# Performance work log

Hardware: AMD Instinct MI355X
Metric: run time of the kernel (lower is better)

The kernel has to match this reference:

```python
import jax, jax.numpy as jnp
import numpy as np

NUM_HEADS = 16


def setup_inputs() -> dict:
    key = jax.random.key(0)
    ks = jax.random.split(key, 5)
    b, s, d = 2, 2048, 1024
    std = (2.0 / (d + d)) ** 0.5
    x = jax.random.normal(ks[0], (b, s, d), dtype=jnp.float32)
    Wq = jax.random.normal(ks[1], (d, d), dtype=jnp.float32) * std
    Wk = jax.random.normal(ks[2], (d, d), dtype=jnp.float32) * std
    Wv = jax.random.normal(ks[3], (d, d), dtype=jnp.float32) * std
    Wo = jax.random.normal(ks[4], (d, d), dtype=jnp.float32) * std
    return {"x": x, "Wq": Wq, "Wk": Wk, "Wv": Wv, "Wo": Wo}


def reference(x, Wq, Wk, Wv, Wo):
    b, s, d = x.shape
    h = NUM_HEADS
    dk = d // h
    # projections: bias-free x @ W (W is [in, out])
    def split_heads(t):
        return t.reshape(b, s, h, dk).transpose(0, 2, 1, 3)  # b h s dk
    q = split_heads(x @ Wq)
    k = split_heads(x @ Wk)
    v = split_heads(x @ Wv)
    scale = 1.0 / jnp.sqrt(jnp.asarray(dk, dtype=x.dtype))
    scores = jnp.einsum('bhqd,bhkd->bhqk', q, k) * scale  # b h s s
    causal = jnp.tril(jnp.ones((s, s), dtype=bool))
    scores = jnp.where(causal, scores, -jnp.inf)
    probs = jax.nn.softmax(scores, axis=-1)
    out = jnp.einsum('bhqk,bhkd->bhqd', probs, v)
    out = out.transpose(0, 2, 1, 3).reshape(b, s, d)  # b s (h dk)
    return out @ Wo
```

## Files before the change

kernel.cpp:

```cpp
#include <hip/hip_runtime.h>

typedef unsigned short u16;
typedef unsigned int   u32;

using bf16x8 = __attribute__((ext_vector_type(8))) __bf16;
using bf16x4 = __attribute__((ext_vector_type(4))) __bf16;
using f32x4  = __attribute__((ext_vector_type(4))) float;
using s16x4  = __attribute__((ext_vector_type(4))) short;

#define NH    16
#define DKH   64
#define SEQ   2048
#define BAT   2
#define DMOD  1024

#define QSCALE 0.18033688011112042f

__device__ __forceinline__ u16 f2bf(float f) {
  union { float f; u32 u; } v; v.f = f;
  u32 r = v.u + 0x7fffu + ((v.u >> 16) & 1u);
  return (u16)(r >> 16);
}

__device__ __forceinline__ u32 pack2bf(float a, float b) {
  union { float f; u32 u; } x, y; x.f = a; y.f = b;
  u32 ua = x.u + 0x7fffu + ((x.u >> 16) & 1u);
  u32 ub = y.u + 0x7fffu + ((y.u >> 16) & 1u);
  return __builtin_amdgcn_perm(ub, ua, 0x07060302u);
}

__device__ __forceinline__ s16x4 pk4bf(float a, float b, float c, float d) {
  union { bf16x4 bv; s16x4 sv; } u;
  u.bv[0] = (__bf16)a; u.bv[1] = (__bf16)b; u.bv[2] = (__bf16)c; u.bv[3] = (__bf16)d;
  return u.sv;
}

#if __has_builtin(__builtin_amdgcn_exp2f)
#define EXP2(x) __builtin_amdgcn_exp2f(x)
#else
#define EXP2(x) exp2f(x)
#endif

#if __has_builtin(__builtin_amdgcn_mfma_f32_16x16x16bf16_1k)
__device__ __forceinline__ f32x4 mfma16(s16x4 a, s16x4 b, f32x4 c) {
  return __builtin_amdgcn_mfma_f32_16x16x16bf16_1k(a, b, c, 0, 0, 0);
}
#else
__device__ __forceinline__ f32x4 mfma16(s16x4 a, s16x4 b, f32x4 c) {
  f32x4 d;
  asm volatile("v_mfma_f32_16x16x16_bf16 %0, %1, %2, %3\n\ts_nop 7\n\ts_nop 7"
               : "=v"(d) : "v"(a), "v"(b), "v"(c));
  return d;
}
#endif

__global__ __launch_bounds__(256) void transpose_all(const float* __restrict__ Wq,
                                                     const float* __restrict__ Wk,
                                                     const float* __restrict__ Wv,
                                                     const float* __restrict__ Wo,
                                                     u16* __restrict__ Wt) {
  __shared__ u16 t[32][33];
  const float* W = blockIdx.z == 0 ? Wq : blockIdx.z == 1 ? Wk : blockIdx.z == 2 ? Wv : Wo;
  u16* o = Wt + (size_t)blockIdx.z * DMOD * DMOD;
  int bx = blockIdx.x * 32, by = blockIdx.y * 32;
  int x = threadIdx.x, y = threadIdx.y;
  #pragma unroll
  for (int i = 0; i < 32; i += 8)
    t[y + i][x] = f2bf(W[(size_t)(by + y + i) * DMOD + bx + x]);
  __syncthreads();
  #pragma unroll
  for (int i = 0; i < 32; i += 8)
    o[(size_t)(bx + y + i) * DMOD + by + x] = t[x][y + i];
}

__global__ __launch_bounds__(256) void convert_x(const float* __restrict__ x,
                                                 u16* __restrict__ xb) {
  size_t i = ((size_t)blockIdx.x * 256 + threadIdx.x) * 8;
  float4 f0 = *(const float4*)(x + i);
  float4 f1 = *(const float4*)(x + i + 4);
  uint4 o;
  o.x = pack2bf(f0.x, f0.y); o.y = pack2bf(f0.z, f0.w);
  o.z = pack2bf(f1.x, f1.y); o.w = pack2bf(f1.z, f1.w);
  *(uint4*)(xb + i) = o;
}

__global__ __launch_bounds__(256, 3) void gemm_qkv(const u16* __restrict__ A,
                                                   const u16* __restrict__ Bt,
                                                   u16* __restrict__ Qo,
                                                   u16* __restrict__ Ko,
                                                   u16* __restrict__ Vo) {
  __shared__ __align__(16) u16 As[128 * 40];
  __shared__ __align__(16) u16 Bs[128 * 40];
  const int tid  = threadIdx.x;
  const int lane = tid & 63, wv = tid >> 6;
  const int wm   = wv >> 1, wn = wv & 1;
  const int lrow = lane & 15, quad = lane >> 4;
  const int tileM = blockIdx.x * 128, tileN = blockIdx.y * 128;
  const int r0 = tid >> 2, c0 = (tid & 3) * 8;
  const int r1 = r0 + 64;

  const f32x4 fz = {0.f, 0.f, 0.f, 0.f};
  f32x4 acc[4][4];
  #pragma unroll
  for (int i = 0; i < 4; ++i)
    #pragma unroll
    for (int j = 0; j < 4; ++j) acc[i][j] = fz;

  uint4 a0 = *(const uint4*)(&A [(size_t)(tileM + r0) * DMOD + c0]);
  uint4 a1 = *(const uint4*)(&A [(size_t)(tileM + r1) * DMOD + c0]);
  uint4 b0 = *(const uint4*)(&Bt[(size_t)(tileN + r0) * DMOD + c0]);
  uint4 b1 = *(const uint4*)(&Bt[(size_t)(tileN + r1) * DMOD + c0]);

  for (int kt = 0; kt < DMOD; kt += 32) {
    __syncthreads();
    *(uint4*)(&As[r0 * 40 + c0]) = a0;
    *(uint4*)(&As[r1 * 40 + c0]) = a1;
    *(uint4*)(&Bs[r0 * 40 + c0]) = b0;
    *(uint4*)(&Bs[r1 * 40 + c0]) = b1;
    if (kt + 32 < DMOD) {
      a0 = *(const uint4*)(&A [(size_t)(tileM + r0) * DMOD + kt + 32 + c0]);
      a1 = *(const uint4*)(&A [(size_t)(tileM + r1) * DMOD + kt + 32 + c0]);
      b0 = *(const uint4*)(&Bt[(size_t)(tileN + r0) * DMOD + kt + 32 + c0]);
      b1 = *(const uint4*)(&Bt[(size_t)(tileN + r1) * DMOD + kt + 32 + c0]);
    }
    __syncthreads();
    bf16x8 af[4], bfr[4];
    #pragma unroll
    for (int mt = 0; mt < 4; ++mt)
      af[mt] = *(const bf16x8*)(&As[(wm * 64 + mt * 16 + lrow) * 40 + quad * 8]);
    #pragma unroll
    for (int nt = 0; nt < 4; ++nt)
      bfr[nt] = *(const bf16x8*)(&Bs[(wn * 64 + nt * 16 + lrow) * 40 + quad * 8]);
    #pragma unroll
    for (int mt = 0; mt < 4; ++mt)
      #pragma unroll
      for (int nt = 0; nt < 4; ++nt)
        acc[mt][nt] = __builtin_amdgcn_mfma_f32_16x16x32_bf16(af[mt], bfr[nt],
                                                              acc[mt][nt], 0, 0, 0);
  }

  #pragma unroll
  for (int mt = 0; mt < 4; ++mt) {
    #pragma unroll
    for (int nt = 0; nt < 4; ++nt) {
      int gm0 = tileM + wm * 64 + mt * 16 + quad * 4;
      int gn  = tileN + wn * 64 + nt * 16 + lrow;
      int which = gn >> 10, col = gn & 1023;
      int bb = gm0 >> 11, srw0 = gm0 & (SEQ - 1);
      int hh = col >> 6, dki = col & (DKH - 1);
      size_t bhi = (size_t)(bb * NH + hh);
      if (which == 0) {
        #pragma unroll
        for (int r = 0; r < 4; ++r)
          Qo[(bhi * SEQ + srw0 + r) * DKH + dki] = f2bf(acc[mt][nt][r] * QSCALE);
      } else if (which == 1) {
        #pragma unroll
        for (int r = 0; r < 4; ++r)
          Ko[(bhi * SEQ + srw0 + r) * DKH + dki] = f2bf(acc[mt][nt][r]);
      } else {
        uint2 pk;
        pk.x = pack2bf(acc[mt][nt][0], acc[mt][nt][1]);
        pk.y = pack2bf(acc[mt][nt][2], acc[mt][nt][3]);
        *(uint2*)(&Vo[(((bhi * (SEQ / 4)) + (srw0 >> 2)) * DKH + dki) * 4]) = pk;
      }
    }
  }
}

__global__ __launch_bounds__(256, 3) void gemm_out(const u16* __restrict__ A,
                                                   const u16* __restrict__ Bt,
                                                   float* __restrict__ Co) {
  __shared__ __align__(16) u16 As[128 * 40];
  __shared__ __align__(16) u16 Bs[64 * 40];
  const int tid  = threadIdx.x;
  const int lane = tid & 63, wv = tid >> 6;
  const int wm   = wv & 1, wn = wv >> 1;
  const int lrow = lane & 15, quad = lane >> 4;
  const int tileM = blockIdx.x * 128, tileN = blockIdx.y * 64;
  const int r0 = tid >> 2, c0 = (tid & 3) * 8;
  const int r1 = r0 + 64;

  const f32x4 fz = {0.f, 0.f, 0.f, 0.f};
  f32x4 acc[4][2];
  #pragma unroll
  for (int i = 0; i < 4; ++i) { acc[i][0] = fz; acc[i][1] = fz; }

  uint4 a0 = *(const uint4*)(&A [(size_t)(tileM + r0) * DMOD + c0]);
  uint4 a1 = *(const uint4*)(&A [(size_t)(tileM + r1) * DMOD + c0]);
  uint4 b0 = *(const uint4*)(&Bt[(size_t)(tileN + (r0 & 63)) * DMOD + c0]);

  for (int kt = 0; kt < DMOD; kt += 32) {
    __syncthreads();
    *(uint4*)(&As[r0 * 40 + c0]) = a0;
    *(uint4*)(&As[r1 * 40 + c0]) = a1;
    if (r0 < 64) *(uint4*)(&Bs[r0 * 40 + c0]) = b0;
    if (kt + 32 < DMOD) {
      a0 = *(const uint4*)(&A [(size_t)(tileM + r0) * DMOD + kt + 32 + c0]);
      a1 = *(const uint4*)(&A [(size_t)(tileM + r1) * DMOD + kt + 32 + c0]);
      b0 = *(const uint4*)(&Bt[(size_t)(tileN + (r0 & 63)) * DMOD + kt + 32 + c0]);
    }
    __syncthreads();
    bf16x8 af[4], bfr[2];
    #pragma unroll
    for (int mt = 0; mt < 4; ++mt)
      af[mt] = *(const bf16x8*)(&As[(wm * 64 + mt * 16 + lrow) * 40 + quad * 8]);
    #pragma unroll
    for (int nt = 0; nt < 2; ++nt)
      bfr[nt] = *(const bf16x8*)(&Bs[(wn * 32 + nt * 16 + lrow) * 40 + quad * 8]);
    #pragma unroll
    for (int mt = 0; mt < 4; ++mt)
      #pragma unroll
      for (int nt = 0; nt < 2; ++nt)
        acc[mt][nt] = __builtin_amdgcn_mfma_f32_16x16x32_bf16(af[mt], bfr[nt],
                                                              acc[mt][nt], 0, 0, 0);
  }

  #pragma unroll
  for (int mt = 0; mt < 4; ++mt)
    #pragma unroll
    for (int nt = 0; nt < 2; ++nt)
      #pragma unroll
      for (int r = 0; r < 4; ++r) {
        int gm = tileM + wm * 64 + mt * 16 + quad * 4 + r;
        int gn = tileN + wn * 32 + nt * 16 + lrow;
        Co[(size_t)gm * DMOD + gn] = acc[mt][nt][r];
      }
}

#define KP 72
#define VP 132
#define OP 68

__global__ __launch_bounds__(128, 2) void attn_k(const u16* __restrict__ Q,
                                                 const u16* __restrict__ Kg,
                                                 const u16* __restrict__ Vg,
                                                 u16* __restrict__ Og) {
  __shared__ __align__(16) u16 Ks[128 * KP];
  __shared__ __align__(16) u16 Vs[64 * VP];

  const int tid  = threadIdx.x;
  const int lane = tid & 63, w = tid >> 6;
  const int lrow = lane & 15, quad = lane >> 4;
  const int bh = blockIdx.x;
  const int t  = blockIdx.y;
  const int qb = (t < 16) ? t : 47 - t;
  const int b = bh >> 4, h = bh & 15;
  const int jmax = qb >> 1;
  const int qoff = qb & 1;

  const u16* Qbh = Q  + (size_t)bh * SEQ * DKH;
  const u16* Kbh = Kg + (size_t)bh * SEQ * DKH;
  const u16* Vbh = Vg + (size_t)bh * SEQ * DKH;

  bf16x8 bq[2][2];
  #pragma unroll
  for (int s = 0; s < 2; ++s)
    #pragma unroll
    for (int kk = 0; kk < 2; ++kk)
      bq[s][kk] = *(const bf16x8*)(&Qbh[(size_t)(qb * 64 + (2 * w + s) * 16 + lrow) * DKH
                                        + kk * 32 + quad * 8]);

  uint4 kreg[8], vreg[8];
  #pragma unroll
  for (int k = 0; k < 8; ++k) {
    int ci = k * 128 + tid;
    kreg[k] = *(const uint4*)(&Kbh[(size_t)(ci >> 3) * DKH + (ci & 7) * 8]);
    vreg[k] = *(const uint4*)(&Vbh[(size_t)(ci >> 5) * 256 + (ci & 31) * 8]);
  }

  const f32x4 fz = {0.f, 0.f, 0.f, 0.f};
  f32x4 oacc[2][4];
  #pragma unroll
  for (int s = 0; s < 2; ++s)
    #pragma unroll
    for (int d = 0; d < 4; ++d) oacc[s][d] = fz;
  float lsum[2] = {0.f, 0.f};

  for (int j = 0; j <= jmax; ++j) {
    if (j) __syncthreads();

    #pragma unroll
    for (int k = 0; k < 8; ++k) {
      int ci = k * 128 + tid;
      *(uint4*)(&Ks[(ci >> 3) * KP + (ci & 7) * 8]) = kreg[k];
      int sq = ci >> 5, dkp = ci & 31;
      union { uint4 q; uint2 d[2]; } vv; vv.q = vreg[k];
      *(uint2*)(&Vs[(2 * dkp)     * VP + 4 * sq]) = vv.d[0];
      *(uint2*)(&Vs[(2 * dkp + 1) * VP + 4 * sq]) = vv.d[1];
    }

    if (j < jmax) {
      const int jn = j + 1;
      #pragma unroll
      for (int k = 0; k < 8; ++k) {
        int ci = k * 128 + tid;
        kreg[k] = *(const uint4*)(&Kbh[(size_t)(jn * 128 + (ci >> 3)) * DKH + (ci & 7) * 8]);
        vreg[k] = *(const uint4*)(&Vbh[(size_t)(jn * 32 + (ci >> 5)) * 256 + (ci & 31) * 8]);
      }
    }

    __syncthreads();

    if (j < jmax) {
      f32x4 sacc[2][8];
      #pragma unroll
      for (int s = 0; s < 2; ++s)
        #pragma unroll
        for (int m = 0; m < 8; ++m) sacc[s][m] = fz;
      #pragma unroll
      for (int kk = 0; kk < 2; ++kk)
        #pragma unroll
        for (int m = 0; m < 8; ++m) {
          bf16x8 ak = *(const bf16x8*)(&Ks[(m * 16 + lrow) * KP + kk * 32 + quad * 8]);
          sacc[0][m] = __builtin_amdgcn_mfma_f32_16x16x32_bf16(ak, bq[0][kk], sacc[0][m], 0, 0, 0);
          sacc[1][m] = __builtin_amdgcn_mfma_f32_16x16x32_bf16(ak, bq[1][kk], sacc[1][m], 0, 0, 0);
        }
      #pragma unroll
      for (int m = 0; m < 8; ++m) {
        float p00 = EXP2(sacc[0][m][0]), p01 = EXP2(sacc[0][m][1]);
        float p02 = EXP2(sacc[0][m][2]), p03 = EXP2(sacc[0][m][3]);
        float p10 = EXP2(sacc[1][m][0]), p11 = EXP2(sacc[1][m][1]);
        float p12 = EXP2(sacc[1][m][2]), p13 = EXP2(sacc[1][m][3]);
        lsum[0] += (p00 + p01) + (p02 + p03);
        lsum[1] += (p10 + p11) + (p12 + p13);
        s16x4 pk0 = pk4bf(p00, p01, p02, p03);
        s16x4 pk1 = pk4bf(p10, p11, p12, p13);
        #pragma unroll
        for (int d = 0; d < 4; ++d) {
          s16x4 av = *(const s16x4*)(&Vs[(d * 16 + lrow) * VP + m * 16 + quad * 4]);
          oacc[0][d] = mfma16(av, pk0, oacc[0][d]);
          oacc[1][d] = mfma16(av, pk1, oacc[1][d]);
        }
      }
    } else {
      #pragma unroll
      for (int s = 0; s < 2; ++s) {
        const int L = qoff * 4 + 2 * w + s;
        for (int m = 0; m < L; ++m) {
          f32x4 sv = fz;
          #pragma unroll
          for (int kk = 0; kk < 2; ++kk) {
            bf16x8 ak = *(const bf16x8*)(&Ks[(m * 16 + lrow) * KP + kk * 32 + quad * 8]);
            sv = __builtin_amdgcn_mfma_f32_16x16x32_bf16(ak, bq[s][kk], sv, 0, 0, 0);
          }
          float p0 = EXP2(sv[0]), p1 = EXP2(sv[1]), p2 = EXP2(sv[2]), p3 = EXP2(sv[3]);
          lsum[s] += (p0 + p1) + (p2 + p3);
          s16x4 pk = pk4bf(p0, p1, p2, p3);
          #pragma unroll
          for (int d = 0; d < 4; ++d) {
            s16x4 av = *(const s16x4*)(&Vs[(d * 16 + lrow) * VP + m * 16 + quad * 4]);
            oacc[s][d] = mfma16(av, pk, oacc[s][d]);
          }
        }
        {
          f32x4 sv = fz;
          #pragma unroll
          for (int kk = 0; kk < 2; ++kk) {
            bf16x8 ak = *(const bf16x8*)(&Ks[(L * 16 + lrow) * KP + kk * 32 + quad * 8]);
            sv = __builtin_amdgcn_mfma_f32_16x16x32_bf16(ak, bq[s][kk], sv, 0, 0, 0);
          }
          float p[4];
          #pragma unroll
          for (int r = 0; r < 4; ++r)
            p[r] = (quad * 4 + r > lrow) ? 0.f : EXP2(sv[r]);
          lsum[s] += (p[0] + p[1]) + (p[2] + p[3]);
          s16x4 pk = pk4bf(p[0], p[1], p[2], p[3]);
          #pragma unroll
          for (int d = 0; d < 4; ++d) {
            s16x4 av = *(const s16x4*)(&Vs[(d * 16 + lrow) * VP + L * 16 + quad * 4]);
            oacc[s][d] = mfma16(av, pk, oacc[s][d]);
          }
        }
      }
    }
  }

  float inv[2];
  #pragma unroll
  for (int s = 0; s < 2; ++s) {
    float ls = lsum[s];
    ls += __shfl_xor(ls, 16, 64);
    ls += __shfl_xor(ls, 32, 64);
    inv[s] = 1.f / ls;
  }

  __syncthreads();
  u16* Osr = Ks;
  #pragma unroll
  for (int s = 0; s < 2; ++s) {
    int row = (2 * w + s) * 16 + lrow;
    #pragma unroll
    for (int d = 0; d < 4; ++d) {
      uint2 pkk;
      pkk.x = pack2bf(oacc[s][d][0] * inv[s], oacc[s][d][1] * inv[s]);
      pkk.y = pack2bf(oacc[s][d][2] * inv[s], oacc[s][d][3] * inv[s]);
      *(uint2*)(&Osr[row * OP + d * 16 + quad * 4]) = pkk;
    }
  }
  __syncthreads();
  #pragma unroll
  for (int k = 0; k < 4; ++k) {
    int c = k * 128 + tid;
    int row = c >> 3, ch = c & 7;
    uint4 v = *(const uint4*)(&Osr[row * OP + ch * 8]);
    *(uint4*)(&Og[(size_t)(b * SEQ + qb * 64 + row) * DMOD + h * DKH + ch * 8]) = v;
  }
}

extern "C" void kernel_launch(void* const* d_in, const int* in_sizes, int n_in,
                              void* d_out, int out_size, void* d_ws, size_t ws_size,
                              hipStream_t stream) {
  const float* x  = (const float*)d_in[0];
  const float* Wq = (const float*)d_in[1];
  const float* Wk = (const float*)d_in[2];
  const float* Wv = (const float*)d_in[3];
  const float* Wo = (const float*)d_in[4];

  u16* ws = (u16*)d_ws;
  const size_t WSZ = (size_t)DMOD * DMOD;
  const size_t TSZ = (size_t)BAT * NH * SEQ * DKH;
  u16* Wt  = ws;
  u16* Wto = Wt + 3 * WSZ;
  u16* xb  = Wt + 4 * WSZ;
  u16* Qb  = xb + TSZ;
  u16* Kb  = Qb + TSZ;
  u16* Vb  = Kb + TSZ;
  u16* Ob  = xb;

  transpose_all<<<dim3(32, 32, 4), dim3(32, 8), 0, stream>>>(Wq, Wk, Wv, Wo, Wt);
  convert_x<<<dim3(2048), 256, 0, stream>>>(x, xb);

  gemm_qkv<<<dim3(32, 24), 256, 0, stream>>>(xb, Wt, Qb, Kb, Vb);

  attn_k<<<dim3(32, 32), 128, 0, stream>>>(Qb, Kb, Vb, Ob);

  gemm_out<<<dim3(32, 16), 256, 0, stream>>>(Ob, Wto, (float*)d_out);
}
```

Measured before the change: 195.1 us.

## Split attention KV range across two blocks with atomic-counter partial merge

```diff
diff --git a/kernel.cpp b/kernel.cpp
--- a/kernel.cpp
+++ b/kernel.cpp
@@ -231,179 +231,217 @@
 #define VP 132
 #define OP 68
 
-__global__ __launch_bounds__(128, 2) void attn_k(const u16* __restrict__ Q,
+__global__ __launch_bounds__(256, 2) void attn_k(const u16* __restrict__ Q,
                                                  const u16* __restrict__ Kg,
                                                  const u16* __restrict__ Vg,
-                                                 u16* __restrict__ Og) {
-  __shared__ __align__(16) u16 Ks[128 * KP];
-  __shared__ __align__(16) u16 Vs[64 * VP];
+                                                 u16* __restrict__ Og,
+                                                 float* __restrict__ Poacc,
+                                                 float* __restrict__ Plsum,
+                                                 u32* __restrict__ Pcnt) {
+  __shared__ __align__(16) u16 KsA[128 * KP];
+  __shared__ __align__(16) u16 VsA[64 * VP];
+  __shared__ __align__(16) u16 KsB[128 * KP];
+  __shared__ __align__(16) u16 VsB[64 * VP];
+  __shared__ u32 flagsh;
 
   const int tid  = threadIdx.x;
   const int lane = tid & 63, w = tid >> 6;
   const int lrow = lane & 15, quad = lane >> 4;
   const int bh = blockIdx.x;
-  const int t  = blockIdx.y;
-  const int qb = (t < 16) ? t : 47 - t;
+  const int y  = blockIdx.y;
+  const int pr  = y & 7;
+  const int par = y >> 3;
   const int b = bh >> 4, h = bh & 15;
-  const int jmax = qb >> 1;
-  const int qoff = qb & 1;
 
   const u16* Qbh = Q  + (size_t)bh * SEQ * DKH;
   const u16* Kbh = Kg + (size_t)bh * SEQ * DKH;
   const u16* Vbh = Vg + (size_t)bh * SEQ * DKH;
 
-  bf16x8 bq[2][2];
-  #pragma unroll
-  for (int s = 0; s < 2; ++s)
-    #pragma unroll
-    for (int kk = 0; kk < 2; ++kk)
-      bq[s][kk] = *(const bf16x8*)(&Qbh[(size_t)(qb * 64 + (2 * w + s) * 16 + lrow) * DKH
-                                        + kk * 32 + quad * 8]);
-
-  uint4 kreg[8], vreg[8];
-  #pragma unroll
-  for (int k = 0; k < 8; ++k) {
-    int ci = k * 128 + tid;
-    kreg[k] = *(const uint4*)(&Kbh[(size_t)(ci >> 3) * DKH + (ci & 7) * 8]);
-    vreg[k] = *(const uint4*)(&Vbh[(size_t)(ci >> 5) * 256 + (ci & 31) * 8]);
-  }
-
   const f32x4 fz = {0.f, 0.f, 0.f, 0.f};
-  f32x4 oacc[2][4];
-  #pragma unroll
-  for (int s = 0; s < 2; ++s)
-    #pragma unroll
-    for (int d = 0; d < 4; ++d) oacc[s][d] = fz;
-  float lsum[2] = {0.f, 0.f};
-
-  for (int j = 0; j <= jmax; ++j) {
-    if (j) __syncthreads();
-
-    #pragma unroll
-    for (int k = 0; k < 8; ++k) {
-      int ci = k * 128 + tid;
-      *(uint4*)(&Ks[(ci >> 3) * KP + (ci & 7) * 8]) = kreg[k];
-      int sq = ci >> 5, dkp = ci & 31;
-      union { uint4 q; uint2 d[2]; } vv; vv.q = vreg[k];
-      *(uint2*)(&Vs[(2 * dkp)     * VP + 4 * sq]) = vv.d[0];
-      *(uint2*)(&Vs[(2 * dkp + 1) * VP + 4 * sq]) = vv.d[1];
-    }
-
-    if (j < jmax) {
-      const int jn = j + 1;
-      #pragma unroll
-      for (int k = 0; k < 8; ++k) {
-        int ci = k * 128 + tid;
-        kreg[k] = *(const uint4*)(&Kbh[(size_t)(jn * 128 + (ci >> 3)) * DKH + (ci & 7) * 8]);
-        vreg[k] = *(const uint4*)(&Vbh[(size_t)(jn * 32 + (ci >> 5)) * 256 + (ci & 31) * 8]);
-      }
-    }
-
-    __syncthreads();
-
-    if (j < jmax) {
-      f32x4 sacc[2][8];
-      #pragma unroll
-      for (int s = 0; s < 2; ++s)
-        #pragma unroll
-        for (int m = 0; m < 8; ++m) sacc[s][m] = fz;
+  int cur = 0;
+
+  for (int half = 0; half < 2; ++half) {
+    const int qt = half ? (15 - pr) : pr;
+
+    bf16x8 bq[2][2];
+    #pragma unroll
+    for (int s = 0; s < 2; ++s)
       #pragma unroll
       for (int kk = 0; kk < 2; ++kk)
+        bq[s][kk] = *(const bf16x8*)(&Qbh[(size_t)(qt * 128 + (2 * w + s) * 16 + lrow) * DKH
+                                          + kk * 32 + quad * 8]);
+
+    f32x4 oacc[2][4];
+    #pragma unroll
+    for (int s = 0; s < 2; ++s)
+      #pragma unroll
+      for (int d = 0; d < 4; ++d) oacc[s][d] = fz;
+    float lsum[2] = {0.f, 0.f};
+
+    uint4 kreg[4], vreg[4];
+    if (par <= qt) {
+      #pragma unroll
+      for (int k = 0; k < 4; ++k) {
+        int ci = k * 256 + tid;
+        kreg[k] = *(const uint4*)(&Kbh[(size_t)(par * 128 + (ci >> 3)) * DKH + (ci & 7) * 8]);
+        vreg[k] = *(const uint4*)(&Vbh[(size_t)(par * 32 + (ci >> 5)) * 256 + (ci & 31) * 8]);
+      }
+    }
+
+    for (int j = par; j <= qt; j += 2) {
+      u16* Ks = cur ? KsB : KsA;
+      u16* Vs = cur ? VsB : VsA;
+
+      #pragma unroll
+      for (int k = 0; k < 4; ++k) {
+        int ci = k * 256 + tid;
+        *(uint4*)(&Ks[(ci >> 3) * KP + (ci & 7) * 8]) = kreg[k];
+        int sq = ci >> 5, dkp = ci & 31;
+        union { uint4 q; uint2 d[2]; } vv; vv.q = vreg[k];
+        *(uint2*)(&Vs[(2 * dkp)     * VP + 4 * sq]) = vv.d[0];
+        *(uint2*)(&Vs[(2 * dkp + 1) * VP + 4 * sq]) = vv.d[1];
+      }
+
+      if (j + 2 <= qt) {
+        const int jn = j + 2;
+        #pragma unroll
+        for (int k = 0; k < 4; ++k) {
+          int ci = k * 256 + tid;
+          kreg[k] = *(const uint4*)(&Kbh[(size_t)(jn * 128 + (ci >> 3)) * DKH + (ci & 7) * 8]);
+          vreg[k] = *(const uint4*)(&Vbh[(size_t)(jn * 32 + (ci >> 5)) * 256 + (ci & 31) * 8]);
+        }
+      }
+
+      __syncthreads();
+
+      if (j < qt) {
         #pragma unroll
         for (int m = 0; m < 8; ++m) {
-          bf16x8 ak = *(const bf16x8*)(&Ks[(m * 16 + lrow) * KP + kk * 32 + quad * 8]);
-          sacc[0][m] = __builtin_amdgcn_mfma_f32_16x16x32_bf16(ak, bq[0][kk], sacc[0][m], 0, 0, 0);
-          sacc[1][m] = __builtin_amdgcn_mfma_f32_16x16x32_bf16(ak, bq[1][kk], sacc[1][m], 0, 0, 0);
-        }
-      #pragma unroll
-      for (int m = 0; m < 8; ++m) {
-        float p00 = EXP2(sacc[0][m][0]), p01 = EXP2(sacc[0][m][1]);
-        float p02 = EXP2(sacc[0][m][2]), p03 = EXP2(sacc[0][m][3]);
-        float p10 = EXP2(sacc[1][m][0]), p11 = EXP2(sacc[1][m][1]);
-        float p12 = EXP2(sacc[1][m][2]), p13 = EXP2(sacc[1][m][3]);
-        lsum[0] += (p00 + p01) + (p02 + p03);
-        lsum[1] += (p10 + p11) + (p12 + p13);
-        s16x4 pk0 = pk4bf(p00, p01, p02, p03);
-        s16x4 pk1 = pk4bf(p10, p11, p12, p13);
-        #pragma unroll
-        for (int d = 0; d < 4; ++d) {
-          s16x4 av = *(const s16x4*)(&Vs[(d * 16 + lrow) * VP + m * 16 + quad * 4]);
-          oacc[0][d] = mfma16(av, pk0, oacc[0][d]);
-          oacc[1][d] = mfma16(av, pk1, oacc[1][d]);
-        }
-      }
-    } else {
-      #pragma unroll
-      for (int s = 0; s < 2; ++s) {
-        const int L = qoff * 4 + 2 * w + s;
-        for (int m = 0; m < L; ++m) {
-          f32x4 sv = fz;
+          f32x4 s0 = fz, s1 = fz;
           #pragma unroll
           for (int kk = 0; kk < 2; ++kk) {
             bf16x8 ak = *(const bf16x8*)(&Ks[(m * 16 + lrow) * KP + kk * 32 + quad * 8]);
-            sv = __builtin_amdgcn_mfma_f32_16x16x32_bf16(ak, bq[s][kk], sv, 0, 0, 0);
+            s0 = __builtin_amdgcn_mfma_f32_16x16x32_bf16(ak, bq[0][kk], s0, 0, 0, 0);
+            s1 = __builtin_amdgcn_mfma_f32_16x16x32_bf16(ak, bq[1][kk], s1, 0, 0, 0);
           }
-          float p0 = EXP2(sv[0]), p1 = EXP2(sv[1]), p2 = EXP2(sv[2]), p3 = EXP2(sv[3]);
-          lsum[s] += (p0 + p1) + (p2 + p3);
-          s16x4 pk = pk4bf(p0, p1, p2, p3);
+          float p00 = EXP2(s0[0]), p01 = EXP2(s0[1]), p02 = EXP2(s0[2]), p03 = EXP2(s0[3]);
+          float p10 = EXP2(s1[0]), p11 = EXP2(s1[1]), p12 = EXP2(s1[2]), p13 = EXP2(s1[3]);
+          lsum[0] += (p00 + p01) + (p02 + p03);
+          lsum[1] += (p10 + p11) + (p12 + p13);
+          s16x4 pk0 = pk4bf(p00, p01, p02, p03);
+          s16x4 pk1 = pk4bf(p10, p11, p12, p13);
           #pragma unroll
           for (int d = 0; d < 4; ++d) {
             s16x4 av = *(const s16x4*)(&Vs[(d * 16 + lrow) * VP + m * 16 + quad * 4]);
-            oacc[s][d] = mfma16(av, pk, oacc[s][d]);
+            oacc[0][d] = mfma16(av, pk0, oacc[0][d]);
+            oacc[1][d] = mfma16(av, pk1, oacc[1][d]);
           }
         }
-        {
-          f32x4 sv = fz;
-          #pragma unroll
-          for (int kk = 0; kk < 2; ++kk) {
-            bf16x8 ak = *(const bf16x8*)(&Ks[(L * 16 + lrow) * KP + kk * 32 + quad * 8]);
-            sv = __builtin_amdgcn_mfma_f32_16x16x32_bf16(ak, bq[s][kk], sv, 0, 0, 0);
+      } else {
+        #pragma unroll
+        for (int s = 0; s < 2; ++s) {
+          const int ss = 2 * w + s;
+          for (int m = 0; m < ss; ++m) {
+            f32x4 sv = fz;
+            #pragma unroll
+            for (int kk = 0; kk < 2; ++kk) {
+              bf16x8 ak = *(const bf16x8*)(&Ks[(m * 16 + lrow) * KP + kk * 32 + quad * 8]);
+              sv = __builtin_amdgcn_mfma_f32_16x16x32_bf16(ak, bq[s][kk], sv, 0, 0, 0);
+            }
+            float p0 = EXP2(sv[0]), p1 = EXP2(sv[1]), p2 = EXP2(sv[2]), p3 = EXP2(sv[3]);
+            lsum[s] += (p0 + p1) + (p2 + p3);
+            s16x4 pk = pk4bf(p0, p1, p2, p3);
+            #pragma unroll
+            for (int d = 0; d < 4; ++d) {
+              s16x4 av = *(const s16x4*)(&Vs[(d * 16 + lrow) * VP + m * 16 + quad * 4]);
+              oacc[s][d] = mfma16(av, pk, oacc[s][d]);
+            }
           }
-          float p[4];
-          #pragma unroll
-          for (int r = 0; r < 4; ++r)
-            p[r] = (quad * 4 + r > lrow) ? 0.f : EXP2(sv[r]);
-          lsum[s] += (p[0] + p[1]) + (p[2] + p[3]);
-          s16x4 pk = pk4bf(p[0], p[1], p[2], p[3]);
-          #pragma unroll
-          for (int d = 0; d < 4; ++d) {
-            s16x4 av = *(const s16x4*)(&Vs[(d * 16 + lrow) * VP + L * 16 + quad * 4]);
-            oacc[s][d] = mfma16(av, pk, oacc[s][d]);
+          {
+            f32x4 sv = fz;
+            #pragma unroll
+            for (int kk = 0; kk < 2; ++kk) {
+              bf16x8 ak = *(const bf16x8*)(&Ks[(ss * 16 + lrow) * KP + kk * 32 + quad * 8]);
+              sv = __builtin_amdgcn_mfma_f32_16x16x32_bf16(ak, bq[s][kk], sv, 0, 0, 0);
+            }
+            float p[4];
+            #pragma unroll
+            for (int r = 0; r < 4; ++r)
+              p[r] = (quad * 4 + r > lrow) ? 0.f : EXP2(sv[r]);
+            lsum[s] += (p[0] + p[1]) + (p[2] + p[3]);
+            s16x4 pk = pk4bf(p[0], p[1], p[2], p[3]);
+            #pragma unroll
+            for (int d = 0; d < 4; ++d) {
+              s16x4 av = *(const s16x4*)(&Vs[(d * 16 + lrow) * VP + ss * 16 + quad * 4]);
+              oacc[s][d] = mfma16(av, pk, oacc[s][d]);
+            }
           }
         }
       }
-    }
-  }
-
-  float inv[2];
-  #pragma unroll
-  for (int s = 0; s < 2; ++s) {
-    float ls = lsum[s];
-    ls += __shfl_xor(ls, 16, 64);
-    ls += __shfl_xor(ls, 32, 64);
-    inv[s] = 1.f / ls;
-  }
-
-  __syncthreads();
-  u16* Osr = Ks;
-  #pragma unroll
-  for (int s = 0; s < 2; ++s) {
-    int row = (2 * w + s) * 16 + lrow;
-    #pragma unroll
-    for (int d = 0; d < 4; ++d) {
-      uint2 pkk;
-      pkk.x = pack2bf(oacc[s][d][0] * inv[s], oacc[s][d][1] * inv[s]);
-      pkk.y = pack2bf(oacc[s][d][2] * inv[s], oacc[s][d][3] * inv[s]);
-      *(uint2*)(&Osr[row * OP + d * 16 + quad * 4]) = pkk;
-    }
-  }
-  __syncthreads();
-  #pragma unroll
-  for (int k = 0; k < 4; ++k) {
-    int c = k * 128 + tid;
-    int row = c >> 3, ch = c & 7;
-    uint4 v = *(const uint4*)(&Osr[row * OP + ch * 8]);
-    *(uint4*)(&Og[(size_t)(b * SEQ + qb * 64 + row) * DMOD + h * DKH + ch * 8]) = v;
+      cur ^= 1;
+    }
+
+    float ls[2];
+    #pragma unroll
+    for (int s = 0; s < 2; ++s) {
+      float v = lsum[s];
+      v += __shfl_xor(v, 16, 64);
+      v += __shfl_xor(v, 32, 64);
+      ls[s] = v;
+    }
+
+    const int tile = bh * 16 + qt;
+    float* myO = Poacc + ((size_t)tile * 2 + par) * (128 * 64);
+    float* myL = Plsum + ((size_t)tile * 2 + par) * 128;
+
+    #pragma unroll
+    for (int s = 0; s < 2; ++s) {
+      int row = (2 * w + s) * 16 + lrow;
+      #pragma unroll
+      for (int d = 0; d < 4; ++d)
+        *(f32x4*)(&myO[row * 64 + d * 16 + quad * 4]) = oacc[s][d];
+      if (quad == 0) myL[row] = ls[s];
+    }
+
+    __syncthreads();
+    if (tid == 0) {
+      __threadfence();
+      flagsh = atomicAdd(&Pcnt[tile], 1);
+    }
+    __syncthreads();
+
+    if (flagsh == 1) {
+      __threadfence();
+      const float* oO = Poacc + ((size_t)tile * 2 + (par ^ 1)) * (128 * 64);
+      const float* oL = Plsum + ((size_t)tile * 2 + (par ^ 1)) * 128;
+      u16* Osr = KsA;
+      #pragma unroll
+      for (int s = 0; s < 2; ++s) {
+        int row = (2 * w + s) * 16 + lrow;
+        float inv = 1.f / (ls[s] + oL[row]);
+        #pragma unroll
+        for (int d = 0; d < 4; ++d) {
+          f32x4 ov = *(const f32x4*)(&oO[row * 64 + d * 16 + quad * 4]);
+          float o0 = (oacc[s][d][0] + ov[0]) * inv;
+          float o1 = (oacc[s][d][1] + ov[1]) * inv;
+          float o2 = (oacc[s][d][2] + ov[2]) * inv;
+          float o3 = (oacc[s][d][3] + ov[3]) * inv;
+          uint2 pkk;
+          pkk.x = pack2bf(o0, o1);
+          pkk.y = pack2bf(o2, o3);
+          *(uint2*)(&Osr[row * OP + d * 16 + quad * 4]) = pkk;
+        }
+      }
+      __syncthreads();
+      #pragma unroll
+      for (int k = 0; k < 4; ++k) {
+        int c = k * 256 + tid;
+        int row = c >> 3, ch = c & 7;
+        uint4 v = *(const uint4*)(&Osr[row * OP + ch * 8]);
+        *(uint4*)(&Og[(size_t)(b * SEQ + qt * 128 + row) * DMOD + h * DKH + ch * 8]) = v;
+      }
+      __syncthreads();
+    }
   }
 }
 
@@ -427,12 +465,19 @@
   u16* Vb  = Kb + TSZ;
   u16* Ob  = xb;
 
+  uintptr_t pp = ((uintptr_t)(Vb + TSZ) + 255) & ~(uintptr_t)255;
+  float* Poacc = (float*)pp;
+  float* Plsum = Poacc + (size_t)512 * 2 * 128 * 64;
+  u32*   Pcnt  = (u32*)(Plsum + (size_t)512 * 2 * 128);
+
+  hipMemsetAsync(Pcnt, 0, 512 * sizeof(u32), stream);
+
   transpose_all<<<dim3(32, 32, 4), dim3(32, 8), 0, stream>>>(Wq, Wk, Wv, Wo, Wt);
   convert_x<<<dim3(2048), 256, 0, stream>>>(x, xb);
 
   gemm_qkv<<<dim3(32, 24), 256, 0, stream>>>(xb, Wt, Qb, Kb, Vb);
 
-  attn_k<<<dim3(32, 32), 128, 0, stream>>>(Qb, Kb, Vb, Ob);
+  attn_k<<<dim3(32, 16), 256, 0, stream>>>(Qb, Kb, Vb, Ob, Poacc, Plsum, Pcnt);
 
   gemm_out<<<dim3(32, 16), 256, 0, stream>>>(Ob, Wto, (float*)d_out);
 }
```

Measured after the change: 287.8 us. +47.5%, slower.
